# Kernel tuning notes

Hardware: AMD Instinct MI355X
Metric: run time of the kernel (lower is better)

## Reference

```python
import jax, jax.numpy as jnp
import numpy as np

BATCH, T, S, M = 512, 4096, 64, 125  # batch, seq_len, n_states, emission alphabet (5^3)


def setup_inputs() -> dict:
    key = jax.random.key(0)
    k1, k2, k3, k4 = jax.random.split(key, 4)
    obs = jax.random.randint(k1, (BATCH, T), 0, M)
    x = jax.nn.one_hot(obs, M, dtype=jnp.float32)            # [B, T, M] one-hot emissions
    I = jax.nn.softmax(jax.random.normal(k2, (1, S)))        # initial state distribution [1, S]
    A = jax.nn.softmax(jax.random.normal(k3, (S, S)), axis=-1)   # transition matrix, rows sum to 1
    Bm = jax.nn.softmax(jax.random.normal(k4, (M, S)), axis=0)   # emission matrix, cols sum to 1
    return {"x": x, "I": I, "A": A, "Bm": Bm}


def reference(x, I, A, Bm):
    """HMM forward algorithm with per-step normalization (default scaling branch of CgpHmmCell).

    Returns the accumulated log-likelihood [B, 1].
    """
    xT = jnp.swapaxes(x, 0, 1)  # [T, B, M] for scan over time

    # t = 1: R = I (broadcast over batch), old_loglik = 0
    E0 = xT[0] @ Bm                                  # [B, S]
    u0 = E0 * I                                      # unscaled alpha
    Z0 = jnp.sum(u0, axis=1, keepdims=True)          # [B, 1]
    carry0 = (u0 / Z0, jnp.log(Z0))

    def step(carry, x_t):
        alpha, ll = carry
        R = alpha @ A                                # [B, S] transition
        E = x_t @ Bm                                 # [B, S] emission lookup (one-hot matmul)
        u = E * R
        Z = jnp.sum(u, axis=1, keepdims=True)        # per-sequence scaling factor
        return (u / Z, ll + jnp.log(Z)), None

    (alpha, loglik), _ = jax.lax.scan(step, carry0, xT[1:])
    return loglik
```

## Files before the change

kernel.cpp:

```cpp
#include <hip/hip_runtime.h>


#define BATCH 512
#define T 4096
#define S 64
#define M 125
#define BMS 68
#define NPACK 10
#define BURNP 2
#define WPB 4
#define RB 56.0f
#define SCALEF 7.205759403792794e16f

typedef __attribute__((ext_vector_type(8))) short bf16x8;
typedef __attribute__((ext_vector_type(4))) float f32x4;
typedef float f32x4u __attribute__((ext_vector_type(4), aligned(4)));

union BFU { unsigned u[4]; bf16x8 v; };

__device__ __forceinline__ unsigned pk_trunc(float a, float b) {
    return (__float_as_uint(b) & 0xFFFF0000u) | (__float_as_uint(a) >> 16);
}
__device__ __forceinline__ unsigned pk_rne(float a, float b) {
    unsigned ua = __float_as_uint(a); ua += 0x7FFFu + ((ua >> 16) & 1u);
    unsigned ub = __float_as_uint(b); ub += 0x7FFFu + ((ub >> 16) & 1u);
    return (ub & 0xFFFF0000u) | (ua >> 16);
}

__global__ __launch_bounds__(256) void hmm_fused(const float* __restrict__ x,
                                                 const float* __restrict__ Iv,
                                                 const float* __restrict__ A,
                                                 const float* __restrict__ Bm,
                                                 float* __restrict__ out) {
    __shared__ __align__(16) float BmL[M * BMS];
    __shared__ __align__(16) float ILds[S];
    __shared__ unsigned long long ulds[WPB * 16 * NPACK];

    const int tid = threadIdx.x, wv = tid >> 6, lane = tid & 63;
    const int s = lane & 15, g = lane >> 4;

    for (int i = tid; i < M * S; i += WPB * 64)
        BmL[(i >> 6) * BMS + (i & 63)] = Bm[i];
    if (tid < S) ILds[tid] = Iv[tid];
    __syncthreads();

    const int W = blockIdx.x * WPB + wv;
    const int seq = W >> 2, wq = W & 3;
    const float* xs = x + (size_t)seq * T * M;
    unsigned long long* myu = &ulds[wv * 16 * NPACK];
    const int base = wq * 1024;

    const int rel = lane & 31, hf = lane >> 5;
    const unsigned coff = (rel < 31) ? 4u * (unsigned)rel : 121u;

    {
        f32x4u bA[8], bB[8], bC[8], bD[8];

        auto issue16 = [&](f32x4u (&bf)[8], int r0a, int r0b) {
#pragma unroll
            for (int j = 0; j < 4; ++j) {
                unsigned ra = (unsigned)((r0a + 2 * j + hf) * 125) + coff;
                unsigned rb = (unsigned)((r0b + 2 * j + hf) * 125) + coff;
                bf[j]     = *(const f32x4u*)&xs[ra];
                bf[4 + j] = *(const f32x4u*)&xs[rb];
            }
        };
        auto ext8 = [&](const f32x4u (&bf)[8], int b) -> unsigned long long {
            unsigned long long acc = 0;
#pragma unroll
            for (int j = 0; j < 4; ++j) {
                f32x4u v = bf[b * 4 + j];
                bool nz = (v.x != 0.f) || (v.y != 0.f) || (v.z != 0.f) || (v.w != 0.f);
                unsigned li = (v.x != 0.f) ? 0u : ((v.y != 0.f) ? 1u : ((v.z != 0.f) ? 2u : 3u));
                unsigned cand = coff + li;
                unsigned long long m = __ballot(nz);
                unsigned l0 = (unsigned)__builtin_ctzll(m & 0xffffffffull);
                unsigned l1 = (unsigned)__builtin_ctzll(m >> 32);
                unsigned o0 = __builtin_amdgcn_readlane(cand, l0);
                unsigned o1 = __builtin_amdgcn_readlane(cand, 32 + l1);
                acc |= ((unsigned long long)o0 << (16 * j)) |
                       ((unsigned long long)o1 << (16 * j + 8));
            }
            return acc;
        };
        auto put = [&](int st, int pt, unsigned long long v) {
            if (lane == st) myu[st * NPACK + pt] = v;
        };
        auto grows = [&](int i, int& r0a, int& r0b) {
            if (i == 0) {
                r0a = base - 16; if (r0a < 0) r0a = 0;
                r0b = base - 8;  if (r0b < 0) r0b = 0;
            } else {
                r0a = base + 16 * (i - 1);
                r0b = r0a + 8;
            }
        };
        auto depq = [&](int q, unsigned long long a) {
            int sc = q >> 3, pos = q & 7;
            put(sc, pos + 2, a);
            if (pos >= 6 && sc < 15) put(sc + 1, pos - 6, a);
        };
        auto dep = [&](int i, unsigned long long a0, unsigned long long a1) {
            if (i == 0) { put(0, 0, a0); put(0, 1, a1); }
            else        { depq(2 * (i - 1), a0); depq(2 * (i - 1) + 1, a1); }
        };

        int ra, rb;
        grows(0, ra, rb); issue16(bA, ra, rb);
        grows(1, ra, rb); issue16(bB, ra, rb);
        grows(2, ra, rb); issue16(bC, ra, rb);
        grows(3, ra, rb); issue16(bD, ra, rb);
        for (int ib = 0; ib < 64; ib += 4) {
            {   unsigned long long a0 = ext8(bA, 0), a1 = ext8(bA, 1);
                if (ib + 4 <= 64) { grows(ib + 4, ra, rb); issue16(bA, ra, rb); }
                dep(ib + 0, a0, a1); }
            {   unsigned long long a0 = ext8(bB, 0), a1 = ext8(bB, 1);
                if (ib + 5 <= 64) { grows(ib + 5, ra, rb); issue16(bB, ra, rb); }
                dep(ib + 1, a0, a1); }
            {   unsigned long long a0 = ext8(bC, 0), a1 = ext8(bC, 1);
                if (ib + 6 <= 64) { grows(ib + 6, ra, rb); issue16(bC, ra, rb); }
                dep(ib + 2, a0, a1); }
            {   unsigned long long a0 = ext8(bD, 0), a1 = ext8(bD, 1);
                if (ib + 7 <= 64) { grows(ib + 7, ra, rb); issue16(bD, ra, rb); }
                dep(ib + 3, a0, a1); }
        }
        {
            unsigned long long a0 = ext8(bA, 0), a1 = ext8(bA, 1);
            dep(64, a0, a1); }
    }

    BFU Af[4][2];
#pragma unroll
    for (int mt = 0; mt < 4; ++mt)
#pragma unroll
        for (int kf = 0; kf < 2; ++kf)
#pragma unroll
            for (int j2 = 0; j2 < 4; ++j2) {
                int p0 = 32 * kf + 16 * (j2 >> 1) + 4 * g + 2 * (j2 & 1);
                Af[mt][kf].u[j2] = pk_rne(A[(size_t)p0 * S + mt * 16 + s],
                                          A[(size_t)(p0 + 1) * S + mt * 16 + s]);
            }

    BFU Bf[2];
#pragma unroll
    for (int kf = 0; kf < 2; ++kf)
#pragma unroll
        for (int j = 0; j < 4; ++j) Bf[kf].u[j] = 0x3F803F80u;

    float S0v = 0.f, swv = 1.f;

    for (int p = 0; p < NPACK; ++p) {
        unsigned long long uv = myu[s * NPACK + p];
#pragma unroll
        for (int k = 0; k < 8; ++k) {
            const int o = (int)(uv & 255ull);
            uv >>= 8;
            const float* br = &BmL[o * BMS];
            f32x4 E[4], z0[4], z1[4];
#pragma unroll
            for (int mt = 0; mt < 4; ++mt) {
                E[mt] = *(const f32x4*)&br[mt * 16 + g * 4];
                f32x4 zr = {0.f, 0.f, 0.f, 0.f};
                z0[mt] = __builtin_amdgcn_mfma_f32_16x16x32_bf16(Af[mt][0].v, Bf[0].v, zr, 0, 0, 0);
                z1[mt] = __builtin_amdgcn_mfma_f32_16x16x32_bf16(Af[mt][1].v, Bf[1].v, zr, 0, 0, 0);
            }
            float w[4][4];
#pragma unroll
            for (int mt = 0; mt < 4; ++mt)
#pragma unroll
                for (int r = 0; r < 4; ++r) w[mt][r] = (z0[mt][r] + z1[mt][r]) * E[mt][r];
            if (p == BURNP && k == 0 && wq == 0) {
                const bool c0 = (s == 0);
#pragma unroll
                for (int mt = 0; mt < 4; ++mt)
#pragma unroll
                    for (int r = 0; r < 4; ++r)
                        w[mt][r] = c0 ? ILds[mt * 16 + g * 4 + r] * E[mt][r] : w[mt][r];
            }
            if (k == 7 && (p == BURNP - 1 || p == NPACK - 1)) {
                float swl = 0.f;
#pragma unroll
                for (int mt = 0; mt < 4; ++mt)
#pragma unroll
                    for (int r = 0; r < 4; ++r) swl += w[mt][r];
                swl += __shfl_xor(swl, 16);
                swl += __shfl_xor(swl, 32);
                swv = swl;
            }
#pragma unroll
            for (int kf = 0; kf < 2; ++kf)
#pragma unroll
                for (int j2 = 0; j2 < 4; ++j2) {
                    int mt = 2 * kf + (j2 >> 1), pr = j2 & 1;
                    float v0 = w[mt][2 * pr], v1 = w[mt][2 * pr + 1];
                    if (k == 7) { v0 *= SCALEF; v1 *= SCALEF; }
                    Bf[kf].u[j2] = pk_trunc(v0, v1);
                }
        }
        if (p == BURNP - 1) {
            const bool ch0 = (wq == 0) && (s == 0);
            S0v = ch0 ? ((float)(NPACK - 1 - BURNP) * RB)
                      : (__log2f(swv) + (float)(NPACK - BURNP) * RB);
        }
    }

    float tot = __log2f(swv) - S0v;
    tot += __shfl_xor(tot, 1);
    tot += __shfl_xor(tot, 2);
    tot += __shfl_xor(tot, 4);
    tot += __shfl_xor(tot, 8);
    if (lane == 0)
        atomicAdd(out + seq, tot * 0.6931471805599453f);
}

extern "C" void kernel_launch(void* const* d_in, const int* in_sizes, int n_in,
                              void* d_out, int out_size, void* d_ws, size_t ws_size,
                              hipStream_t stream) {
    const float* x  = (const float*)d_in[0];
    const float* I  = (const float*)d_in[1];
    const float* A  = (const float*)d_in[2];
    const float* Bm = (const float*)d_in[3];
    float* out = (float*)d_out;
    (void)d_ws; (void)ws_size;

    hipMemsetAsync(out, 0, (size_t)out_size * sizeof(float), stream);
    hmm_fused<<<(BATCH * 4) / WPB, WPB * 64, 0, stream>>>(x, I, A, Bm, out);
}
```

Before: 1.323 ms.

## Split waves into observation-decode producers and recurrence consumers with LDS flags

Each block now holds two producer waves that scan the one-hot input and pack observation indices into LDS, and two consumer waves that run the MFMA recurrence. Consumers spin on per-pack LDS flags rather than waiting for the whole decode to finish, so decode of later packs overlaps compute of earlier ones. The decode order is reshuffled so the packs each consumer needs first are produced first. The grid is doubled and launch bounds request 4 blocks per CU. In exchange, half the waves do no recurrence work, and the spin-wait relies on LDS ordering through lgkmcnt waits and volatile stores.

```diff
diff --git a/kernel.cpp b/kernel.cpp
--- a/kernel.cpp
+++ b/kernel.cpp
@@ -8,7 +8,6 @@
 #define BMS 68
 #define NPACK 10
 #define BURNP 2
-#define WPB 4
 #define RB 56.0f
 #define SCALEF 7.205759403792794e16f
 
@@ -27,49 +26,52 @@
     return (ub & 0xFFFF0000u) | (ua >> 16);
 }
 
-__global__ __launch_bounds__(256) void hmm_fused(const float* __restrict__ x,
-                                                 const float* __restrict__ Iv,
-                                                 const float* __restrict__ A,
-                                                 const float* __restrict__ Bm,
-                                                 float* __restrict__ out) {
+__global__ __launch_bounds__(256, 4) void hmm_fused(const float* __restrict__ x,
+                                                    const float* __restrict__ Iv,
+                                                    const float* __restrict__ A,
+                                                    const float* __restrict__ Bm,
+                                                    float* __restrict__ out) {
     __shared__ __align__(16) float BmL[M * BMS];
     __shared__ __align__(16) float ILds[S];
-    __shared__ unsigned long long ulds[WPB * 16 * NPACK];
+    __shared__ unsigned long long ulds[2 * 16 * NPACK];
+    __shared__ unsigned fl[2 * NPACK];
 
     const int tid = threadIdx.x, wv = tid >> 6, lane = tid & 63;
     const int s = lane & 15, g = lane >> 4;
 
-    for (int i = tid; i < M * S; i += WPB * 64)
+    for (int i = tid; i < M * S; i += 256)
         BmL[(i >> 6) * BMS + (i & 63)] = Bm[i];
     if (tid < S) ILds[tid] = Iv[tid];
+    if (tid < 2 * NPACK) fl[tid] = 0u;
     __syncthreads();
 
-    const int W = blockIdx.x * WPB + wv;
-    const int seq = W >> 2, wq = W & 3;
+    const int h = blockIdx.x & 1, seq = blockIdx.x >> 1;
+    const int j = wv & 1;
+    const int wq = 2 * h + j;
+    const int base = wq * 1024;
     const float* xs = x + (size_t)seq * T * M;
-    unsigned long long* myu = &ulds[wv * 16 * NPACK];
-    const int base = wq * 1024;
+    unsigned long long* myu = &ulds[j * 16 * NPACK];
 
     const int rel = lane & 31, hf = lane >> 5;
     const unsigned coff = (rel < 31) ? 4u * (unsigned)rel : 121u;
 
-    {
-        f32x4u bA[8], bB[8], bC[8], bD[8];
+    if (wv < 2) {
+        f32x4u bA[8], bB[8], bC[8];
 
         auto issue16 = [&](f32x4u (&bf)[8], int r0a, int r0b) {
 #pragma unroll
-            for (int j = 0; j < 4; ++j) {
-                unsigned ra = (unsigned)((r0a + 2 * j + hf) * 125) + coff;
-                unsigned rb = (unsigned)((r0b + 2 * j + hf) * 125) + coff;
-                bf[j]     = *(const f32x4u*)&xs[ra];
-                bf[4 + j] = *(const f32x4u*)&xs[rb];
+            for (int jj = 0; jj < 4; ++jj) {
+                unsigned ra = (unsigned)((r0a + 2 * jj + hf) * 125) + coff;
+                unsigned rb = (unsigned)((r0b + 2 * jj + hf) * 125) + coff;
+                bf[jj]     = *(const f32x4u*)&xs[ra];
+                bf[4 + jj] = *(const f32x4u*)&xs[rb];
             }
         };
         auto ext8 = [&](const f32x4u (&bf)[8], int b) -> unsigned long long {
             unsigned long long acc = 0;
 #pragma unroll
-            for (int j = 0; j < 4; ++j) {
-                f32x4u v = bf[b * 4 + j];
+            for (int jj = 0; jj < 4; ++jj) {
+                f32x4u v = bf[b * 4 + jj];
                 bool nz = (v.x != 0.f) || (v.y != 0.f) || (v.z != 0.f) || (v.w != 0.f);
                 unsigned li = (v.x != 0.f) ? 0u : ((v.y != 0.f) ? 1u : ((v.z != 0.f) ? 2u : 3u));
                 unsigned cand = coff + li;
@@ -78,55 +80,72 @@
                 unsigned l1 = (unsigned)__builtin_ctzll(m >> 32);
                 unsigned o0 = __builtin_amdgcn_readlane(cand, l0);
                 unsigned o1 = __builtin_amdgcn_readlane(cand, 32 + l1);
-                acc |= ((unsigned long long)o0 << (16 * j)) |
-                       ((unsigned long long)o1 << (16 * j + 8));
+                acc |= ((unsigned long long)o0 << (16 * jj)) |
+                       ((unsigned long long)o1 << (16 * jj + 8));
             }
             return acc;
         };
         auto put = [&](int st, int pt, unsigned long long v) {
             if (lane == st) myu[st * NPACK + pt] = v;
         };
-        auto grows = [&](int i, int& r0a, int& r0b) {
-            if (i == 0) {
+        auto grows = [&](int gx, int& r0a, int& r0b) {
+            if (gx == 0) {
                 r0a = base - 16; if (r0a < 0) r0a = 0;
                 r0b = base - 8;  if (r0b < 0) r0b = 0;
+            } else if (gx <= 8) {
+                int i = gx - 1; r0a = base + 128 * i + 48; r0b = base + 128 * i + 112;
+            } else if (gx <= 16) {
+                int i = gx - 9; r0a = base + 128 * i + 56; r0b = base + 128 * i + 120;
             } else {
-                r0a = base + 16 * (i - 1);
-                r0b = r0a + 8;
-            }
-        };
-        auto depq = [&](int q, unsigned long long a) {
-            int sc = q >> 3, pos = q & 7;
-            put(sc, pos + 2, a);
-            if (pos >= 6 && sc < 15) put(sc + 1, pos - 6, a);
-        };
-        auto dep = [&](int i, unsigned long long a0, unsigned long long a1) {
-            if (i == 0) { put(0, 0, a0); put(0, 1, a1); }
-            else        { depq(2 * (i - 1), a0); depq(2 * (i - 1) + 1, a1); }
+                int b = gx - 17; int pb2 = b >> 3, si = 2 * (b & 7);
+                r0a = base + 64 * si + 8 * pb2; r0b = r0a + 64;
+            }
+        };
+        auto dep = [&](int gx, unsigned long long a0, unsigned long long a1) {
+            if (gx == 0) { put(0, 0, a0); put(0, 1, a1); }
+            else if (gx <= 8) { int i = gx - 1;
+                put(2 * i, 8, a0);     put(2 * i + 1, 0, a0);
+                put(2 * i + 1, 8, a1); if (2 * i + 2 < 16) put(2 * i + 2, 0, a1);
+            } else if (gx <= 16) { int i = gx - 9;
+                put(2 * i, 9, a0);     put(2 * i + 1, 1, a0);
+                put(2 * i + 1, 9, a1); if (2 * i + 2 < 16) put(2 * i + 2, 1, a1);
+            } else { int b = gx - 17; int p = (b >> 3) + 2, si = 2 * (b & 7);
+                put(si, p, a0); put(si + 1, p, a1);
+            }
+        };
+        auto flg = [&](int gx) {
+            int f0 = -1, f1 = -1;
+            if (gx == 8)       { f0 = 0; f1 = 8; }
+            else if (gx == 16) { f0 = 1; f1 = 9; }
+            else if (gx >= 24 && (gx & 7) == 0) f0 = 2 + ((gx - 24) >> 3);
+            if (f0 >= 0) {
+                asm volatile("s_waitcnt lgkmcnt(0)" ::: "memory");
+                if (lane == 0) {
+                    *(volatile unsigned*)&fl[j * NPACK + f0] = 1u;
+                    if (f1 >= 0) *(volatile unsigned*)&fl[j * NPACK + f1] = 1u;
+                }
+            }
         };
 
         int ra, rb;
         grows(0, ra, rb); issue16(bA, ra, rb);
         grows(1, ra, rb); issue16(bB, ra, rb);
         grows(2, ra, rb); issue16(bC, ra, rb);
-        grows(3, ra, rb); issue16(bD, ra, rb);
-        for (int ib = 0; ib < 64; ib += 4) {
-            {   unsigned long long a0 = ext8(bA, 0), a1 = ext8(bA, 1);
-                if (ib + 4 <= 64) { grows(ib + 4, ra, rb); issue16(bA, ra, rb); }
-                dep(ib + 0, a0, a1); }
-            {   unsigned long long a0 = ext8(bB, 0), a1 = ext8(bB, 1);
-                if (ib + 5 <= 64) { grows(ib + 5, ra, rb); issue16(bB, ra, rb); }
-                dep(ib + 1, a0, a1); }
-            {   unsigned long long a0 = ext8(bC, 0), a1 = ext8(bC, 1);
-                if (ib + 6 <= 64) { grows(ib + 6, ra, rb); issue16(bC, ra, rb); }
-                dep(ib + 2, a0, a1); }
-            {   unsigned long long a0 = ext8(bD, 0), a1 = ext8(bD, 1);
-                if (ib + 7 <= 64) { grows(ib + 7, ra, rb); issue16(bD, ra, rb); }
-                dep(ib + 3, a0, a1); }
+        for (int gb = 0; gb < 65; gb += 3) {
+            {   const int gx = gb;
+                unsigned long long a0 = ext8(bA, 0), a1 = ext8(bA, 1);
+                if (gx + 3 <= 64) { grows(gx + 3, ra, rb); issue16(bA, ra, rb); }
+                dep(gx, a0, a1); flg(gx); }
+            if (gb + 1 <= 64) { const int gx = gb + 1;
+                unsigned long long a0 = ext8(bB, 0), a1 = ext8(bB, 1);
+                if (gx + 3 <= 64) { grows(gx + 3, ra, rb); issue16(bB, ra, rb); }
+                dep(gx, a0, a1); flg(gx); }
+            if (gb + 2 <= 64) { const int gx = gb + 2;
+                unsigned long long a0 = ext8(bC, 0), a1 = ext8(bC, 1);
+                if (gx + 3 <= 64) { grows(gx + 3, ra, rb); issue16(bC, ra, rb); }
+                dep(gx, a0, a1); flg(gx); }
         }
-        {
-            unsigned long long a0 = ext8(bA, 0), a1 = ext8(bA, 1);
-            dep(64, a0, a1); }
+        return;
     }
 
     BFU Af[4][2];
@@ -145,11 +164,14 @@
 #pragma unroll
     for (int kf = 0; kf < 2; ++kf)
 #pragma unroll
-        for (int j = 0; j < 4; ++j) Bf[kf].u[j] = 0x3F803F80u;
+        for (int jj = 0; jj < 4; ++jj) Bf[kf].u[jj] = 0x3F803F80u;
 
     float S0v = 0.f, swv = 1.f;
+    volatile unsigned* flj = &fl[j * NPACK];
 
     for (int p = 0; p < NPACK; ++p) {
+        while (flj[p] == 0u) __builtin_amdgcn_s_sleep(2);
+        asm volatile("" ::: "memory");
         unsigned long long uv = myu[s * NPACK + p];
 #pragma unroll
         for (int k = 0; k < 8; ++k) {
@@ -224,5 +246,5 @@
     (void)d_ws; (void)ws_size;
 
     hipMemsetAsync(out, 0, (size_t)out_size * sizeof(float), stream);
-    hmm_fused<<<(BATCH * 4) / WPB, WPB * 64, 0, stream>>>(x, I, A, Bm, out);
-}
+    hmm_fused<<<BATCH * 2, 256, 0, stream>>>(x, I, A, Bm, out);
+}
```

Result: no change. 1.304 ms (-1.5%).
